# Kernel tuning notes

Measured on AMD Instinct MI355X. Metric: run time of the kernel, lower is better.

Reference implementation:

```python
import jax, jax.numpy as jnp
import numpy as np

# dims matching init_kwargs / input_specs
N, C, H, W = 8, 256, 64, 64
OUT_C, KH, KW = 256, 3, 3
STRIDE, PAD = 1, 1
OUT_H = (H - KH + 2 * PAD) // STRIDE + 1  # 64
OUT_W = (W - KW + 2 * PAD) // STRIDE + 1  # 64
K = KH * KW


def setup_inputs() -> dict:
    key = jax.random.key(0)
    k1, k2, k3 = jax.random.split(key, 3)
    x = jax.random.normal(k1, (N, C, H, W), dtype=jnp.float32)
    offset = jax.random.normal(k2, (N, 2 * K, OUT_H, OUT_W), dtype=jnp.float32)
    # kaiming-uniform-ish scale for weight (fan_in = C*KH*KW)
    bound = 1.0 / np.sqrt(C * KH * KW)
    weight = jax.random.uniform(k3, (OUT_C, C, KH, KW), dtype=jnp.float32,
                                minval=-bound, maxval=bound)
    return {"input": x, "offset": offset, "weight": weight}


def _deform_conv(x, offset, weight):
    # base sampling positions in pixel coords: y = oy*stride + ky - pad
    ky = jnp.repeat(jnp.arange(KH, dtype=jnp.float32) - PAD, KW)  # [K]
    kx = jnp.tile(jnp.arange(KW, dtype=jnp.float32) - PAD, KH)    # [K]
    oy = jnp.arange(OUT_H, dtype=jnp.float32) * STRIDE            # [outH]
    ox = jnp.arange(OUT_W, dtype=jnp.float32) * STRIDE            # [outW]
    base_y = ky[:, None, None] + oy[None, :, None]  # [K, outH, 1]
    base_x = kx[:, None, None] + ox[None, None, :]  # [K, 1, outW]

    off = offset.reshape(N, K, 2, OUT_H, OUT_W)
    y = base_y[None] + off[:, :, 0]  # [N, K, outH, outW], offset channel 0 = dy
    xp = base_x[None] + off[:, :, 1]  # channel 1 = dx

    # bilinear sample with zero padding (grid_sample align_corners=True, zeros)
    y0 = jnp.floor(y)
    x0 = jnp.floor(xp)
    bidx = jnp.arange(N)[:, None, None, None]
    acc = jnp.zeros((N, K, OUT_H, OUT_W, C), dtype=x.dtype)
    for dy in (0.0, 1.0):
        for dx in (0.0, 1.0):
            yi = y0 + dy
            xi = x0 + dx
            wgt = (1.0 - jnp.abs(y - yi)) * (1.0 - jnp.abs(xp - xi))
            valid = ((yi >= 0) & (yi <= H - 1) & (xi >= 0) & (xi <= W - 1))
            yc = jnp.clip(yi, 0, H - 1).astype(jnp.int32)
            xc = jnp.clip(xi, 0, W - 1).astype(jnp.int32)
            g = x[bidx, :, yc, xc]  # [N, K, outH, outW, C]
            acc = acc + g * (wgt * valid.astype(x.dtype))[..., None]

    # weight.view(outC, -1) flattens (C, KH, KW) -> (C, K) ordering
    w = weight.reshape(OUT_C, C, K)
    out = jnp.einsum('nkhwc,ock->nohw', acc, w)  # [N, outC, outH, outW]
    return out


def reference(input, offset, weight):
    # NOTE: original forward never adds bias -> faithfully omitted
    return _deform_conv(input, offset, weight)
```

## Files before the change

kernel.cpp:

```cpp
#include <hip/hip_runtime.h>
#include <hip/hip_fp16.h>
#include <stdint.h>


typedef _Float16 half8 __attribute__((ext_vector_type(8)));
typedef float f32x4 __attribute__((ext_vector_type(4)));

__device__ __forceinline__ __half2 h2(uint32_t u) {
  return __builtin_bit_cast(__half2, u);
}
__device__ __forceinline__ uint32_t packh2f(float a, float b) {
  return __builtin_bit_cast(uint32_t, __floats2half2_rn(a, b));
}
__device__ __forceinline__ __half2 duplo(uint32_t u) {
  return __half2half2(__builtin_bit_cast(__half, (unsigned short)(u & 0xffffu)));
}
__device__ __forceinline__ __half2 duphi(uint32_t u) {
  return __half2half2(__builtin_bit_cast(__half, (unsigned short)(u >> 16)));
}

__global__ __launch_bounds__(256) void prep_all_kernel(
    const float* __restrict__ x, const float* __restrict__ w,
    const float* __restrict__ offset,
    unsigned short* __restrict__ xb, unsigned short* __restrict__ w3s,
    unsigned short* __restrict__ coords) {
  __shared__ float tile[64][65];
  int tid = threadIdx.x;
  if (blockIdx.x < 2048) {
    int bn   = blockIdx.x >> 8;
    int rem  = blockIdx.x & 255;
    int y    = rem >> 2;
    int cblk = rem & 3;
    const float* src = x + ((size_t)(bn * 256 + cblk * 64)) * 4096 + y * 64;
#pragma unroll
    for (int i = 0; i < 4; ++i) {
      int u  = i * 256 + tid;
      int cl = u >> 4;
      int xs = (u & 15) * 4;
      float4 v = *(const float4*)(src + cl * 4096 + xs);
      tile[cl][xs] = v.x; tile[cl][xs + 1] = v.y;
      tile[cl][xs + 2] = v.z; tile[cl][xs + 3] = v.w;
    }
    __syncthreads();
    unsigned short* dst = xb + ((size_t)(bn * 64 + y) * 64) * 256 + cblk * 64;
#pragma unroll
    for (int i = 0; i < 8; ++i) {
      int v2  = i * 256 + tid;
      int xc  = v2 >> 5;
      int cl2 = (v2 & 31) * 2;
      *(uint32_t*)(dst + xc * 256 + cl2) = packh2f(tile[cl2][xc], tile[cl2 + 1][xc]);
    }
  } else if (blockIdx.x < 4352) {
    int idx = (blockIdx.x - 2048) * 256 + tid;
    int t   = idx >> 14;
    int r2  = idx & 16383;
    int g   = r2 >> 3;
    int e   = r2 & 7;
    int oc  = g >> 3;
    int kk8 = (g & 7) ^ (oc & 7);
    int kk  = kk8 * 8 + e;
    int c   = (t & 3) * 64 + kk;
    int k   = t >> 2;
    w3s[idx] = __builtin_bit_cast(unsigned short, __float2half(w[(oc * 256 + c) * 9 + k]));
  } else {
    int idx = (blockIdx.x - 4352) * 256 + tid;
    int ow  = idx & 63;
    int oh  = (idx >> 6) & 63;
    int r   = idx >> 12;
    int k   = r % 9;
    int bn  = r / 9;
    int ky = k / 3 - 1;
    int kx = k % 3 - 1;
    float offy = offset[((bn * 18 + 2 * k    ) * 64 + oh) * 64 + ow];
    float offx = offset[((bn * 18 + 2 * k + 1) * 64 + oh) * 64 + ow];
    float y = (float)(oh + ky) + offy;
    float x2 = (float)(ow + kx) + offx;
    float y0f = floorf(y), x0f = floorf(x2);
    float fy = y - y0f, fx = x2 - x0f;
    int y0 = (int)y0f, x0 = (int)x0f;
    int y1 = y0 + 1, x1 = x0 + 1;
    float vy0 = (y0 >= 0 && y0 <= 63) ? 1.0f : 0.0f;
    float vy1 = (y1 >= 0 && y1 <= 63) ? 1.0f : 0.0f;
    float vx0 = (x0 >= 0 && x0 <= 63) ? 1.0f : 0.0f;
    float vx1 = (x1 >= 0 && x1 <= 63) ? 1.0f : 0.0f;
    float wy0 = (1.0f - fy) * vy0, wy1 = fy * vy1;
    float wx0 = (1.0f - fx) * vx0, wx1 = fx * vx1;
    int y0c = min(max(y0, 0), 63), y1c = min(max(y1, 0), 63);
    int x0c = min(max(x0, 0), 63), x1c = min(max(x1, 0), 63);
    unsigned short ent[8];
    ent[0] = __builtin_bit_cast(unsigned short, __float2half(wy0 * wx0));
    ent[1] = __builtin_bit_cast(unsigned short, __float2half(wy0 * wx1));
    ent[2] = __builtin_bit_cast(unsigned short, __float2half(wy1 * wx0));
    ent[3] = __builtin_bit_cast(unsigned short, __float2half(wy1 * wx1));
    ent[4] = (unsigned short)(y0c * 64 + x0c);
    ent[5] = (unsigned short)(y0c * 64 + x1c);
    ent[6] = (unsigned short)(y1c * 64 + x0c);
    ent[7] = (unsigned short)(y1c * 64 + x1c);
    *(uint4*)(coords + (size_t)idx * 8) = *(const uint4*)ent;
  }
}

__global__ __launch_bounds__(512, 2) void deform_mfma_kernel(
    const unsigned short* __restrict__ xb,
    const unsigned short* __restrict__ coords,
    const unsigned short* __restrict__ w3s,
    float* __restrict__ out) {
  __shared__ __align__(16) unsigned short At[2][128 * 64];

  int bn  = blockIdx.x & 7;
  int ohp = blockIdx.x >> 3;
  int tid = threadIdx.x;

  int w    = tid >> 6;
  int lane = tid & 63;
  int wrow = w & 1;
  int wcol = w >> 1;
  int mrow = lane & 15;
  int quad = lane >> 4;

  int srow = tid >> 3;
  int sg   = tid & 7;

  const char* xbc = (const char*)(xb + (size_t)bn * (64 * 64 * 256));
  const unsigned short* cb0 = coords + ((size_t)((bn * 9) * 64 + ohp * 2) * 64 + srow) * 8;
  const unsigned short* cb1 = cb0 + 512;

  int aw0 = srow * 64 + ((sg ^ (srow & 7)) * 8);
  int grp0 = quad ^ (mrow & 7);
  int grp1 = (4 + quad) ^ (mrow & 7);
  int a_off0 = (wrow * 64 + mrow) * 64 + grp0 * 8;
  int a_off1 = (wrow * 64 + mrow) * 64 + grp1 * 8;
  int boff0 = ((wcol * 64 + mrow) * 8 + grp0) * 16;
  int boff1 = ((wcol * 64 + mrow) * 8 + grp1) * 16;

  f32x4 acc[4][4] = {};
  half8 bA[2][4], bB[2][4];

  __half2 w00, w01, w02, w03, w10, w11, w12, w13;
  uint32_t o00, o01, o02, o03, o10, o11, o12, o13;
  uint4 cn0, cn1;

#define BLOADR(TT, BS)                                                          \
  {                                                                             \
    const char* wp = (const char*)w3s + (size_t)(TT) * 32768;                   \
    _Pragma("unroll")                                                           \
    for (int nn = 0; nn < 4; ++nn) {                                            \
      BS[0][nn] = *(const half8*)(wp + boff0 + nn * 2048);                      \
      BS[1][nn] = *(const half8*)(wp + boff1 + nn * 2048);                      \
    }                                                                           \
  }

#define TAPSETUP_R(CE0, CE1)                                                    \
  {                                                                             \
    w00 = duplo((CE0).x); w01 = duphi((CE0).x);                                 \
    w02 = duplo((CE0).y); w03 = duphi((CE0).y);                                 \
    o00 = (((CE0).z & 0xffffu) << 9) + sg * 16;                                 \
    o01 = (((CE0).z >> 16) << 9) + sg * 16;                                     \
    o02 = (((CE0).w & 0xffffu) << 9) + sg * 16;                                 \
    o03 = (((CE0).w >> 16) << 9) + sg * 16;                                     \
    w10 = duplo((CE1).x); w11 = duphi((CE1).x);                                 \
    w12 = duplo((CE1).y); w13 = duphi((CE1).y);                                 \
    o10 = (((CE1).z & 0xffffu) << 9) + sg * 16;                                 \
    o11 = (((CE1).z >> 16) << 9) + sg * 16;                                     \
    o12 = (((CE1).w & 0xffffu) << 9) + sg * 16;                                 \
    o13 = (((CE1).w >> 16) << 9) + sg * 16;                                     \
  }

#define ASTAGE(TT, ATP)                                                         \
  {                                                                             \
    {                                                                           \
      uint4 c0 = *(const uint4*)(xbc + o00 + ((TT) & 3) * 128);                 \
      uint4 c1 = *(const uint4*)(xbc + o01 + ((TT) & 3) * 128);                 \
      uint4 c2 = *(const uint4*)(xbc + o02 + ((TT) & 3) * 128);                 \
      uint4 c3 = *(const uint4*)(xbc + o03 + ((TT) & 3) * 128);                 \
      __half2 r0 = __hmul2(h2(c0.x), w00);                                      \
      r0 = __hfma2(h2(c1.x), w01, r0); r0 = __hfma2(h2(c2.x), w02, r0);         \
      r0 = __hfma2(h2(c3.x), w03, r0);                                          \
      __half2 r1 = __hmul2(h2(c0.y), w00);                                      \
      r1 = __hfma2(h2(c1.y), w01, r1); r1 = __hfma2(h2(c2.y), w02, r1);         \
      r1 = __hfma2(h2(c3.y), w03, r1);                                          \
      __half2 r2 = __hmul2(h2(c0.z), w00);                                      \
      r2 = __hfma2(h2(c1.z), w01, r2); r2 = __hfma2(h2(c2.z), w02, r2);         \
      r2 = __hfma2(h2(c3.z), w03, r2);                                          \
      __half2 r3 = __hmul2(h2(c0.w), w00);                                      \
      r3 = __hfma2(h2(c1.w), w01, r3); r3 = __hfma2(h2(c2.w), w02, r3);         \
      r3 = __hfma2(h2(c3.w), w03, r3);                                          \
      uint4 pk;                                                                 \
      pk.x = __builtin_bit_cast(uint32_t, r0);                                  \
      pk.y = __builtin_bit_cast(uint32_t, r1);                                  \
      pk.z = __builtin_bit_cast(uint32_t, r2);                                  \
      pk.w = __builtin_bit_cast(uint32_t, r3);                                  \
      *(uint4*)((ATP) + aw0) = pk;                                              \
    }                                                                           \
    {                                                                           \
      uint4 c0 = *(const uint4*)(xbc + o10 + ((TT) & 3) * 128);                 \
      uint4 c1 = *(const uint4*)(xbc + o11 + ((TT) & 3) * 128);                 \
      uint4 c2 = *(const uint4*)(xbc + o12 + ((TT) & 3) * 128);                 \
      uint4 c3 = *(const uint4*)(xbc + o13 + ((TT) & 3) * 128);                 \
      __half2 r0 = __hmul2(h2(c0.x), w10);                                      \
      r0 = __hfma2(h2(c1.x), w11, r0); r0 = __hfma2(h2(c2.x), w12, r0);         \
      r0 = __hfma2(h2(c3.x), w13, r0);                                          \
      __half2 r1 = __hmul2(h2(c0.y), w10);                                      \
      r1 = __hfma2(h2(c1.y), w11, r1); r1 = __hfma2(h2(c2.y), w12, r1);         \
      r1 = __hfma2(h2(c3.y), w13, r1);                                          \
      __half2 r2 = __hmul2(h2(c0.z), w10);                                      \
      r2 = __hfma2(h2(c1.z), w11, r2); r2 = __hfma2(h2(c2.z), w12, r2);         \
      r2 = __hfma2(h2(c3.z), w13, r2);                                          \
      __half2 r3 = __hmul2(h2(c0.w), w10);                                      \
      r3 = __hfma2(h2(c1.w), w11, r3); r3 = __hfma2(h2(c2.w), w12, r3);         \
      r3 = __hfma2(h2(c3.w), w13, r3);                                          \
      uint4 pk;                                                                 \
      pk.x = __builtin_bit_cast(uint32_t, r0);                                  \
      pk.y = __builtin_bit_cast(uint32_t, r1);                                  \
      pk.z = __builtin_bit_cast(uint32_t, r2);                                  \
      pk.w = __builtin_bit_cast(uint32_t, r3);                                  \
      *(uint4*)((ATP) + aw0 + 4096) = pk;                                       \
    }                                                                           \
  }

#define COMPUTE(ATP, BS)                                                        \
  {                                                                             \
    _Pragma("unroll")                                                           \
    for (int m = 0; m < 4; ++m) {                                               \
      half8 af0 = *(const half8*)((ATP) + a_off0 + m * 1024);                   \
      half8 af1 = *(const half8*)((ATP) + a_off1 + m * 1024);                   \
      _Pragma("unroll")                                                         \
      for (int nn = 0; nn < 4; ++nn) {                                          \
        acc[m][nn] = __builtin_amdgcn_mfma_f32_16x16x32_f16(af0, BS[0][nn], acc[m][nn], 0, 0, 0); \
        acc[m][nn] = __builtin_amdgcn_mfma_f32_16x16x32_f16(af1, BS[1][nn], acc[m][nn], 0, 0, 0); \
      }                                                                         \
    }                                                                           \
  }

  {
    uint4 ce0 = *(const uint4*)cb0;
    uint4 ce1 = *(const uint4*)cb1;
    TAPSETUP_R(ce0, ce1)
  }
  BLOADR(0, bA)
  ASTAGE(0, &At[0][0])
  __syncthreads();

  for (int tap = 0; tap < 9; ++tap) {
#pragma unroll
    for (int cc = 0; cc < 4; ++cc) {
      const int t = tap * 4 + cc;
      if (t < 35) {
        if (cc & 1) { BLOADR(t + 1, bA) } else { BLOADR(t + 1, bB) }
        if (cc == 2 && tap < 8) {
          cn0 = *(const uint4*)(cb0 + (tap + 1) * 32768);
          cn1 = *(const uint4*)(cb1 + (tap + 1) * 32768);
        }
        if (cc == 3) TAPSETUP_R(cn0, cn1)
        if (cc & 1) { ASTAGE(t + 1, &At[0][0]) } else { ASTAGE(t + 1, &At[1][0]) }
      }
      if (cc & 1) { COMPUTE(&At[1][0], bB) } else { COMPUTE(&At[0][0], bA) }
      __syncthreads();
    }
  }

  float* outp = out + (size_t)bn * 256 * 4096 + (size_t)(ohp * 2 + wrow) * 64;
#pragma unroll
  for (int m = 0; m < 4; ++m) {
    int ow0 = m * 16 + quad * 4;
#pragma unroll
    for (int nn = 0; nn < 4; ++nn) {
      int oc = wcol * 64 + nn * 16 + mrow;
      *(f32x4*)(outp + (size_t)oc * 4096 + ow0) = acc[m][nn];
    }
  }
#undef BLOADR
#undef TAPSETUP_R
#undef ASTAGE
#undef COMPUTE
}

extern "C" void kernel_launch(void* const* d_in, const int* in_sizes, int n_in,
                              void* d_out, int out_size, void* d_ws, size_t ws_size,
                              hipStream_t stream) {
  (void)in_sizes; (void)n_in; (void)out_size; (void)ws_size;
  const float* x      = (const float*)d_in[0];
  const float* offset = (const float*)d_in[1];
  const float* weight = (const float*)d_in[2];
  float* out = (float*)d_out;

  unsigned short* xb     = (unsigned short*)d_ws;
  unsigned short* w3s    = xb + (size_t)8 * 64 * 64 * 256;
  unsigned short* coords = w3s + (size_t)36 * 16384;

  prep_all_kernel<<<5504, 256, 0, stream>>>(x, weight, offset, xb, w3s, coords);
  deform_mfma_kernel<<<256, 512, 0, stream>>>(xb, coords, w3s, out);
}
```

Before: 144.8 us.

## Halve block M-tile to one output row, doubling grid and occupancy

```diff
diff --git a/kernel.cpp b/kernel.cpp
--- a/kernel.cpp
+++ b/kernel.cpp
@@ -100,15 +100,15 @@
   }
 }
 
-__global__ __launch_bounds__(512, 2) void deform_mfma_kernel(
+__global__ __launch_bounds__(512, 4) void deform_mfma_kernel(
     const unsigned short* __restrict__ xb,
     const unsigned short* __restrict__ coords,
     const unsigned short* __restrict__ w3s,
     float* __restrict__ out) {
-  __shared__ __align__(16) unsigned short At[2][128 * 64];
+  __shared__ __align__(16) unsigned short At[2][64 * 64];
 
   int bn  = blockIdx.x & 7;
-  int ohp = blockIdx.x >> 3;
+  int oh  = blockIdx.x >> 3;
   int tid = threadIdx.x;
 
   int w    = tid >> 6;
@@ -122,23 +122,21 @@
   int sg   = tid & 7;
 
   const char* xbc = (const char*)(xb + (size_t)bn * (64 * 64 * 256));
-  const unsigned short* cb0 = coords + ((size_t)((bn * 9) * 64 + ohp * 2) * 64 + srow) * 8;
-  const unsigned short* cb1 = cb0 + 512;
-
-  int aw0 = srow * 64 + ((sg ^ (srow & 7)) * 8);
+  const unsigned short* cb = coords + ((size_t)((bn * 9) * 64 + oh) * 64 + srow) * 8;
+
+  int aw0  = srow * 64 + ((sg ^ (srow & 7)) * 8);
   int grp0 = quad ^ (mrow & 7);
   int grp1 = (4 + quad) ^ (mrow & 7);
-  int a_off0 = (wrow * 64 + mrow) * 64 + grp0 * 8;
-  int a_off1 = (wrow * 64 + mrow) * 64 + grp1 * 8;
+  int a_base = (wrow * 32 + mrow) * 64;
   int boff0 = ((wcol * 64 + mrow) * 8 + grp0) * 16;
   int boff1 = ((wcol * 64 + mrow) * 8 + grp1) * 16;
 
-  f32x4 acc[4][4] = {};
+  f32x4 acc[2][4] = {};
   half8 bA[2][4], bB[2][4];
 
-  __half2 w00, w01, w02, w03, w10, w11, w12, w13;
-  uint32_t o00, o01, o02, o03, o10, o11, o12, o13;
-  uint4 cn0, cn1;
+  __half2 w00, w01, w02, w03;
+  uint32_t o00, o01, o02, o03;
+  uint4 cn;
 
 #define BLOADR(TT, BS)                                                          \
   {                                                                             \
@@ -150,80 +148,48 @@
     }                                                                           \
   }
 
-#define TAPSETUP_R(CE0, CE1)                                                    \
-  {                                                                             \
-    w00 = duplo((CE0).x); w01 = duphi((CE0).x);                                 \
-    w02 = duplo((CE0).y); w03 = duphi((CE0).y);                                 \
-    o00 = (((CE0).z & 0xffffu) << 9) + sg * 16;                                 \
-    o01 = (((CE0).z >> 16) << 9) + sg * 16;                                     \
-    o02 = (((CE0).w & 0xffffu) << 9) + sg * 16;                                 \
-    o03 = (((CE0).w >> 16) << 9) + sg * 16;                                     \
-    w10 = duplo((CE1).x); w11 = duphi((CE1).x);                                 \
-    w12 = duplo((CE1).y); w13 = duphi((CE1).y);                                 \
-    o10 = (((CE1).z & 0xffffu) << 9) + sg * 16;                                 \
-    o11 = (((CE1).z >> 16) << 9) + sg * 16;                                     \
-    o12 = (((CE1).w & 0xffffu) << 9) + sg * 16;                                 \
-    o13 = (((CE1).w >> 16) << 9) + sg * 16;                                     \
+#define TAPSETUP_R(CE)                                                          \
+  {                                                                             \
+    w00 = duplo((CE).x); w01 = duphi((CE).x);                                   \
+    w02 = duplo((CE).y); w03 = duphi((CE).y);                                   \
+    o00 = (((CE).z & 0xffffu) << 9) + sg * 16;                                  \
+    o01 = (((CE).z >> 16) << 9) + sg * 16;                                      \
+    o02 = (((CE).w & 0xffffu) << 9) + sg * 16;                                  \
+    o03 = (((CE).w >> 16) << 9) + sg * 16;                                      \
   }
 
 #define ASTAGE(TT, ATP)                                                         \
   {                                                                             \
-    {                                                                           \
-      uint4 c0 = *(const uint4*)(xbc + o00 + ((TT) & 3) * 128);                 \
-      uint4 c1 = *(const uint4*)(xbc + o01 + ((TT) & 3) * 128);                 \
-      uint4 c2 = *(const uint4*)(xbc + o02 + ((TT) & 3) * 128);                 \
-      uint4 c3 = *(const uint4*)(xbc + o03 + ((TT) & 3) * 128);                 \
-      __half2 r0 = __hmul2(h2(c0.x), w00);                                      \
-      r0 = __hfma2(h2(c1.x), w01, r0); r0 = __hfma2(h2(c2.x), w02, r0);         \
-      r0 = __hfma2(h2(c3.x), w03, r0);                                          \
-      __half2 r1 = __hmul2(h2(c0.y), w00);                                      \
-      r1 = __hfma2(h2(c1.y), w01, r1); r1 = __hfma2(h2(c2.y), w02, r1);         \
-      r1 = __hfma2(h2(c3.y), w03, r1);                                          \
-      __half2 r2 = __hmul2(h2(c0.z), w00);                                      \
-      r2 = __hfma2(h2(c1.z), w01, r2); r2 = __hfma2(h2(c2.z), w02, r2);         \
-      r2 = __hfma2(h2(c3.z), w03, r2);                                          \
-      __half2 r3 = __hmul2(h2(c0.w), w00);                                      \
-      r3 = __hfma2(h2(c1.w), w01, r3); r3 = __hfma2(h2(c2.w), w02, r3);         \
-      r3 = __hfma2(h2(c3.w), w03, r3);                                          \
-      uint4 pk;                                                                 \
-      pk.x = __builtin_bit_cast(uint32_t, r0);                                  \
-      pk.y = __builtin_bit_cast(uint32_t, r1);                                  \
-      pk.z = __builtin_bit_cast(uint32_t, r2);                                  \
-      pk.w = __builtin_bit_cast(uint32_t, r3);                                  \
-      *(uint4*)((ATP) + aw0) = pk;                                              \
-    }                                                                           \
-    {                                                                           \
-      uint4 c0 = *(const uint4*)(xbc + o10 + ((TT) & 3) * 128);                 \
-      uint4 c1 = *(const uint4*)(xbc + o11 + ((TT) & 3) * 128);                 \
-      uint4 c2 = *(const uint4*)(xbc + o12 + ((TT) & 3) * 128);                 \
-      uint4 c3 = *(const uint4*)(xbc + o13 + ((TT) & 3) * 128);                 \
-      __half2 r0 = __hmul2(h2(c0.x), w10);                                      \
-      r0 = __hfma2(h2(c1.x), w11, r0); r0 = __hfma2(h2(c2.x), w12, r0);         \
-      r0 = __hfma2(h2(c3.x), w13, r0);                                          \
-      __half2 r1 = __hmul2(h2(c0.y), w10);                                      \
-      r1 = __hfma2(h2(c1.y), w11, r1); r1 = __hfma2(h2(c2.y), w12, r1);         \
-      r1 = __hfma2(h2(c3.y), w13, r1);                                          \
-      __half2 r2 = __hmul2(h2(c0.z), w10);                                      \
-      r2 = __hfma2(h2(c1.z), w11, r2); r2 = __hfma2(h2(c2.z), w12, r2);         \
-      r2 = __hfma2(h2(c3.z), w13, r2);                                          \
-      __half2 r3 = __hmul2(h2(c0.w), w10);                                      \
-      r3 = __hfma2(h2(c1.w), w11, r3); r3 = __hfma2(h2(c2.w), w12, r3);         \
-      r3 = __hfma2(h2(c3.w), w13, r3);                                          \
-      uint4 pk;                                                                 \
-      pk.x = __builtin_bit_cast(uint32_t, r0);                                  \
-      pk.y = __builtin_bit_cast(uint32_t, r1);                                  \
-      pk.z = __builtin_bit_cast(uint32_t, r2);                                  \
-      pk.w = __builtin_bit_cast(uint32_t, r3);                                  \
-      *(uint4*)((ATP) + aw0 + 4096) = pk;                                       \
-    }                                                                           \
+    uint4 c0 = *(const uint4*)(xbc + o00 + ((TT) & 3) * 128);                   \
+    uint4 c1 = *(const uint4*)(xbc + o01 + ((TT) & 3) * 128);                   \
+    uint4 c2 = *(const uint4*)(xbc + o02 + ((TT) & 3) * 128);                   \
+    uint4 c3 = *(const uint4*)(xbc + o03 + ((TT) & 3) * 128);                   \
+    __half2 r0 = __hmul2(h2(c0.x), w00);                                        \
+    r0 = __hfma2(h2(c1.x), w01, r0); r0 = __hfma2(h2(c2.x), w02, r0);           \
+    r0 = __hfma2(h2(c3.x), w03, r0);                                            \
+    __half2 r1 = __hmul2(h2(c0.y), w00);                                        \
+    r1 = __hfma2(h2(c1.y), w01, r1); r1 = __hfma2(h2(c2.y), w02, r1);           \
+    r1 = __hfma2(h2(c3.y), w03, r1);                                            \
+    __half2 r2 = __hmul2(h2(c0.z), w00);                                        \
+    r2 = __hfma2(h2(c1.z), w01, r2); r2 = __hfma2(h2(c2.z), w02, r2);           \
+    r2 = __hfma2(h2(c3.z), w03, r2);                                            \
+    __half2 r3 = __hmul2(h2(c0.w), w00);                                        \
+    r3 = __hfma2(h2(c1.w), w01, r3); r3 = __hfma2(h2(c2.w), w02, r3);           \
+    r3 = __hfma2(h2(c3.w), w03, r3);                                            \
+    uint4 pk;                                                                   \
+    pk.x = __builtin_bit_cast(uint32_t, r0);                                    \
+    pk.y = __builtin_bit_cast(uint32_t, r1);                                    \
+    pk.z = __builtin_bit_cast(uint32_t, r2);                                    \
+    pk.w = __builtin_bit_cast(uint32_t, r3);                                    \
+    *(uint4*)((ATP) + aw0) = pk;                                                \
   }
 
 #define COMPUTE(ATP, BS)                                                        \
   {                                                                             \
     _Pragma("unroll")                                                           \
-    for (int m = 0; m < 4; ++m) {                                               \
-      half8 af0 = *(const half8*)((ATP) + a_off0 + m * 1024);                   \
-      half8 af1 = *(const half8*)((ATP) + a_off1 + m * 1024);                   \
+    for (int m = 0; m < 2; ++m) {                                               \
+      half8 af0 = *(const half8*)((ATP) + a_base + m * 1024 + grp0 * 8);        \
+      half8 af1 = *(const half8*)((ATP) + a_base + m * 1024 + grp1 * 8);        \
       _Pragma("unroll")                                                         \
       for (int nn = 0; nn < 4; ++nn) {                                          \
         acc[m][nn] = __builtin_amdgcn_mfma_f32_16x16x32_f16(af0, BS[0][nn], acc[m][nn], 0, 0, 0); \
@@ -233,9 +199,8 @@
   }
 
   {
-    uint4 ce0 = *(const uint4*)cb0;
-    uint4 ce1 = *(const uint4*)cb1;
-    TAPSETUP_R(ce0, ce1)
+    uint4 ce0 = *(const uint4*)cb;
+    TAPSETUP_R(ce0)
   }
   BLOADR(0, bA)
   ASTAGE(0, &At[0][0])
@@ -247,11 +212,8 @@
       const int t = tap * 4 + cc;
       if (t < 35) {
         if (cc & 1) { BLOADR(t + 1, bA) } else { BLOADR(t + 1, bB) }
-        if (cc == 2 && tap < 8) {
-          cn0 = *(const uint4*)(cb0 + (tap + 1) * 32768);
-          cn1 = *(const uint4*)(cb1 + (tap + 1) * 32768);
-        }
-        if (cc == 3) TAPSETUP_R(cn0, cn1)
+        if (cc == 2 && tap < 8) cn = *(const uint4*)(cb + (tap + 1) * 32768);
+        if (cc == 3) TAPSETUP_R(cn)
         if (cc & 1) { ASTAGE(t + 1, &At[0][0]) } else { ASTAGE(t + 1, &At[1][0]) }
       }
       if (cc & 1) { COMPUTE(&At[1][0], bB) } else { COMPUTE(&At[0][0], bA) }
@@ -259,10 +221,10 @@
     }
   }
 
-  float* outp = out + (size_t)bn * 256 * 4096 + (size_t)(ohp * 2 + wrow) * 64;
-#pragma unroll
-  for (int m = 0; m < 4; ++m) {
-    int ow0 = m * 16 + quad * 4;
+  float* outp = out + (size_t)bn * 256 * 4096 + (size_t)oh * 64;
+#pragma unroll
+  for (int m = 0; m < 2; ++m) {
+    int ow0 = wrow * 32 + m * 16 + quad * 4;
 #pragma unroll
     for (int nn = 0; nn < 4; ++nn) {
       int oc = wcol * 64 + nn * 16 + mrow;
@@ -289,5 +251,5 @@
   unsigned short* coords = w3s + (size_t)36 * 16384;
 
   prep_all_kernel<<<5504, 256, 0, stream>>>(x, weight, offset, xb, w3s, coords);
-  deform_mfma_kernel<<<256, 512, 0, stream>>>(xb, coords, w3s, out);
-}
+  deform_mfma_kernel<<<512, 512, 0, stream>>>(xb, coords, w3s, out);
+}
```

New measurement: 197.9 us. +36.7%, slower.
